# Optimization experiments

Hardware: AMD Instinct MI355X
Metric: run time of the kernel (lower is better)

The kernel has to match this reference:

```python
import jax, jax.numpy as jnp
import numpy as np
from functools import partial

TAU = 2.0          # leak
VTH = 1.0          # threshold_value
DECAY = 1.0 - 1.0 / TAU  # decay_input=False, v_reset=0: v = v*(1-1/tau) + x
PAD = 3
STRIDE = 1


def heaviside(x):
    # forward of spikingjelly surrogate.ATan (surrogate only changes backward)
    return (x >= 0).astype(x.dtype)


def lif(v, inp):
    """One LIF step: charge, fire, hard reset (v_reset=0)."""
    v = v * DECAY + inp
    s = heaviside(v - VTH)
    v = v * (1.0 - s)
    return v, s


def setup_inputs() -> dict:
    key = jax.random.key(0)
    k1, k2, k3, k4 = jax.random.split(key, 4)
    B, L = 64, 2048
    C, H, NC, K = 128, 256, 10, 7
    x = jax.random.normal(k1, (B, L), dtype=jnp.float32)
    conv_w = jax.random.normal(k2, (C, 1, K), dtype=jnp.float32) * (1.0 / np.sqrt(K))
    W1 = jax.random.normal(k3, (H, C), dtype=jnp.float32) * (1.0 / np.sqrt(C))
    W2 = jax.random.normal(k4, (NC, H), dtype=jnp.float32) * (1.0 / np.sqrt(H))
    return {"x": x, "conv_w": conv_w, "W1": W1, "W2": W2}


def _forward(x, conv_w, W1, W2):
    B = x.shape[0]
    C, H, NC = conv_w.shape[0], W1.shape[0], W2.shape[0]
    # Conv1d(1 -> C): [B, 1, L] -> [B, C, T]
    xc = jax.lax.conv_general_dilated(
        x[:, None, :], conv_w, window_strides=(STRIDE,),
        padding=[(PAD, PAD)], dimension_numbers=("NCH", "OIH", "NCH"))
    T = xc.shape[2]
    xt = jnp.transpose(xc, (2, 0, 1))  # [T, B, C]

    def step(carry, x_t):
        v1, v2, v3, acc = carry
        v1, s1 = lif(v1, x_t)                       # conv LIF  [B, C]
        v2, s2 = lif(v2, s1 @ W1.T)                 # hidden LIF [B, H]
        v3, s3 = lif(v3, s2 @ W2.T)                 # output LIF [B, NC]
        return (v1, v2, v3, acc + s3), None

    zeros = lambda d: jnp.zeros((B, d), dtype=x.dtype)
    init = (zeros(C), zeros(H), zeros(NC), zeros(NC))
    (_, _, _, acc), _ = jax.lax.scan(step, init, xt)
    return acc / T


def reference(x, conv_w, W1, W2):
    return _forward(x, conv_w, W1, W2)
```

## Files before the change

### kernel.cpp

```cpp
#include <hip/hip_runtime.h>
#include <stdint.h>

#define T_STEPS 2048
#define BB 64
#define CC 128
#define HH 256
#define NCLS 10

#define S1_OFF  0
#define DP_OFF  2097152
#define DP2_OFF 2228224
#define S2W_OFF 2244608

typedef int v4i __attribute__((ext_vector_type(4)));

__device__ __forceinline__ v4i spread16(unsigned h) {
  v4i a;
  a[0] = (int)((((h      ) & 0xFu) * 0x00204081u) & 0x01010101u);
  a[1] = (int)((((h >> 4 ) & 0xFu) * 0x00204081u) & 0x01010101u);
  a[2] = (int)((((h >> 8 ) & 0xFu) * 0x00204081u) & 0x01010101u);
  a[3] = (int)((((h >> 12) & 0xFu) * 0x00204081u) & 0x01010101u);
  return a;
}

__global__ __launch_bounds__(128) void k01_prep(
    const float* __restrict__ x, const float* __restrict__ cw,
    const float* __restrict__ W1, const float* __restrict__ W2,
    unsigned int* __restrict__ s1b, signed char* __restrict__ dp,
    signed char* __restrict__ dp2, float* __restrict__ out) {
  const int bx = blockIdx.x;
  const int tidx = threadIdx.x;
  __shared__ float xs[200];

  if (bx < 1024) {
    const int c = tidx;
    const int wv = tidx >> 6;
    const int lane = tidx & 63;
    const int b = bx & 63;
    const int t0 = (bx >> 6) * 128;
    const int ts = t0 - 64;

    const float* xb = x + b * 2048;
    const int base = t0 - 67;
    for (int i = tidx; i < 200; i += 128) {
      int l = base + i;
      xs[i] = (l >= 0 && l < 2048) ? xb[l] : 0.0f;
    }
    __syncthreads();

    float w[7];
#pragma unroll
    for (int k = 0; k < 7; ++k) w[k] = cw[c * 7 + k];

    float xw[7];
#pragma unroll
    for (int k = 0; k < 7; ++k) xw[k] = xs[k];

    float v = 0.0f;
#pragma unroll 7
    for (int t = ts; t < t0 + 128; ++t) {
      float u = fmaf(w[0], xw[0],
                fmaf(w[1], xw[1],
                fmaf(w[2], xw[2],
                fmaf(w[3], xw[3],
                fmaf(w[4], xw[4],
                fmaf(w[5], xw[5], w[6] * xw[6]))))));
      v = fmaf(v, 0.5f, u);
      bool sp = (v >= 1.0f);
      unsigned long long Bm = __ballot(sp);
      if (t >= t0 && lane == 0)
        *(unsigned long long*)(s1b + ((size_t)t * BB + b) * 4 + wv * 2) = Bm;
      if (sp) v = 0.0f;
#pragma unroll
      for (int k = 0; k < 6; ++k) xw[k] = xw[k + 1];
      xw[6] = xs[t - t0 + 71];
    }
  } else if (bx < 1280) {
    const int h = bx - 1024;
    const int c = tidx;
    float w = W1[h * CC + c];
    int q = __float2int_rn(w * 2147483648.0f);
#pragma unroll
    for (int d = 0; d < 3; ++d) {
      int dig = (int)(signed char)(q & 0xff);
      dp[d * (HH * CC) + h * CC + c] = (signed char)dig;
      q = (q - dig) >> 8;
    }
    dp[3 * (HH * CC) + h * CC + c] = (signed char)q;
  } else if (bx < 1296) {
    const int nc = bx - 1280;
#pragma unroll
    for (int half = 0; half < 2; ++half) {
      int cc = half * 128 + tidx;
      float w = (nc < NCLS) ? W2[nc * HH + cc] : 0.0f;
      int q = __float2int_rn(w * 2147483648.0f);
#pragma unroll
      for (int d = 0; d < 3; ++d) {
        int dig = (int)(signed char)(q & 0xff);
        dp2[d * (16 * HH) + nc * HH + cc] = (signed char)dig;
        q = (q - dig) >> 8;
      }
      dp2[3 * (16 * HH) + nc * HH + cc] = (signed char)q;
    }
  } else {
#pragma unroll
    for (int i = 0; i < 5; ++i) out[tidx + 128 * i] = 0.0f;
  }
}

__global__ __launch_bounds__(256, 4) void k2_mfma_lif2(
    const unsigned int* __restrict__ s1b, const signed char* __restrict__ dp,
    unsigned int* __restrict__ s2w) {
  const int tid  = threadIdx.x;
  const int lane = tid & 63;
  const int wv   = tid >> 6;
  const int hg   = blockIdx.x;
  const int b    = blockIdx.y;
  const int chunk= blockIdx.z;
  const int t0   = chunk * 256;
  const int nwarm= (chunk == 0) ? 0 : 4;
  const int ts   = t0 - nwarm * 16;
  const int l15  = lane & 15;
  const int lg   = lane >> 4;
  const int nn   = lg >> 1;
  const int hb   = hg * 128 + wv * 32;
  const int hw   = (lg & 1) * 16;

  v4i Bf[2][4][2];
#pragma unroll
  for (int n = 0; n < 2; ++n)
#pragma unroll
    for (int d = 0; d < 4; ++d)
#pragma unroll
      for (int kc = 0; kc < 2; ++kc)
        Bf[n][d][kc] = *(const v4i*)(dp + d * (HH * CC) +
                                     (hb + n * 16 + l15) * CC + kc * 64 + lg * 16);

  const unsigned int* ap = s1b + ((size_t)(ts + l15) * BB + b) * 4;
  uint4 Ra = *(const uint4*)ap;
  uint4 Pb = *(const uint4*)(ap + 16 * BB * 4);
  const unsigned int* ap2 = ap + 2 * 16 * BB * 4;

  const int a4 = l15 * 4;
  float v = 0.0f;
  const v4i ZZ = {0, 0, 0, 0};

  const int nsub = nwarm + 16;
  for (int s = 0; s < nsub; ++s) {
    const int tb = ts + s * 16;

    uint4 Pc = *(const uint4*)ap2;
    ap2 += 16 * BB * 4;

    const unsigned w01 = (lg & 2) ? Ra.y : Ra.x;
    const unsigned w23 = (lg & 2) ? Ra.w : Ra.z;
    v4i Af0 = spread16((w01 >> hw) & 0xFFFFu);
    v4i Af1 = spread16((w23 >> hw) & 0xFFFFu);

    float u0[4], u1[4];
#pragma unroll
    for (int n = 0; n < 2; ++n) {
      v4i a0, a1, a2, a3;
      a0 = __builtin_amdgcn_mfma_i32_16x16x64_i8(Af0, Bf[n][0][0], ZZ, 0, 0, 0);
      a1 = __builtin_amdgcn_mfma_i32_16x16x64_i8(Af0, Bf[n][1][0], ZZ, 0, 0, 0);
      a2 = __builtin_amdgcn_mfma_i32_16x16x64_i8(Af0, Bf[n][2][0], ZZ, 0, 0, 0);
      a3 = __builtin_amdgcn_mfma_i32_16x16x64_i8(Af0, Bf[n][3][0], ZZ, 0, 0, 0);
      a0 = __builtin_amdgcn_mfma_i32_16x16x64_i8(Af1, Bf[n][0][1], a0, 0, 0, 0);
      a1 = __builtin_amdgcn_mfma_i32_16x16x64_i8(Af1, Bf[n][1][1], a1, 0, 0, 0);
      a2 = __builtin_amdgcn_mfma_i32_16x16x64_i8(Af1, Bf[n][2][1], a2, 0, 0, 0);
      a3 = __builtin_amdgcn_mfma_i32_16x16x64_i8(Af1, Bf[n][3][1], a3, 0, 0, 0);
#pragma unroll
      for (int r = 0; r < 4; ++r) {
        int hi = a3[r] * 256 + a2[r];
        int lo = a1[r] * 256 + a0[r];
        float u = fmaf((float)hi, 0x1p-15f, (float)lo * 0x1p-31f);
        if (n == 0) u0[r] = u; else u1[r] = u;
      }
    }

    float ua[16];
#pragma unroll
    for (int q = 0; q < 4; ++q) {
      const int addr = a4 + q * 64;
#pragma unroll
      for (int r = 0; r < 4; ++r) {
        int g0 = __builtin_amdgcn_ds_bpermute(addr, __float_as_int(u0[r]));
        int g1 = __builtin_amdgcn_ds_bpermute(addr, __float_as_int(u1[r]));
        ua[q * 4 + r] = __int_as_float(nn ? g1 : g0);
      }
    }

    unsigned sel = 0;
#define LIFSTEP(J)                                                         \
    {                                                                      \
      v = fmaf(v, 0.5f, ua[J]);                                            \
      bool sp = (v >= 1.0f);                                               \
      if (sp) v = 0.0f;                                                    \
      unsigned long long Bm = __ballot(sp);                                \
      unsigned pk = (unsigned)(Bm & 0xFFFFull) |                           \
                    ((unsigned)((Bm >> 32) & 0xFFFFull) << 16);            \
      asm("v_writelane_b32 %0, %1, " #J : "+v"(sel) : "s"(pk));            \
    }
    LIFSTEP(0)  LIFSTEP(1)  LIFSTEP(2)  LIFSTEP(3)
    LIFSTEP(4)  LIFSTEP(5)  LIFSTEP(6)  LIFSTEP(7)
    LIFSTEP(8)  LIFSTEP(9)  LIFSTEP(10) LIFSTEP(11)
    LIFSTEP(12) LIFSTEP(13) LIFSTEP(14) LIFSTEP(15)
#undef LIFSTEP

    if (s >= nwarm && lg == 0)
      s2w[((size_t)(tb + l15) * BB + b) * 8 + hg * 4 + wv] = sel;

    Ra = Pb; Pb = Pc;
  }
}

__global__ __launch_bounds__(64, 4) void k34_gemm3_lif3(
    const unsigned int* __restrict__ s2w, const signed char* __restrict__ dp2,
    float* __restrict__ out) {
  const int lane = threadIdx.x;
  const int l15  = lane & 15;
  const int lg   = lane >> 4;
  const int b    = blockIdx.x;
  const int chunk= blockIdx.y;
  const int t0   = chunk * 32;
  const int nwarm= (chunk == 0) ? 0 : 4;
  const int ts   = t0 - nwarm * 16;

  v4i Bf[4][4];
#pragma unroll
  for (int d = 0; d < 4; ++d)
#pragma unroll
    for (int kc = 0; kc < 4; ++kc)
      Bf[d][kc] = *(const v4i*)(dp2 + d * (16 * HH) + l15 * HH + kc * 64 + lg * 16);

  const uint4* rp = (const uint4*)s2w + ((size_t)(ts + l15) * BB + b) * 2;
  uint4 r0 = rp[0], r1 = rp[1];
  rp += 16 * BB * 2;

  const int a4 = l15 * 4;
  const int hw = (lg & 1) * 16;
  float v = 0.0f, cnt = 0.0f;
  const v4i ZZ = {0, 0, 0, 0};

  const int nsub = nwarm + 2;
  for (int s = 0; s < nsub; ++s) {
    uint4 p0 = rp[0], p1 = rp[1];
    rp += 16 * BB * 2;

    unsigned rowd[8] = {r0.x, r0.y, r0.z, r0.w, r1.x, r1.y, r1.z, r1.w};

    v4i a0, a1, a2, a3;
#pragma unroll
    for (int kc = 0; kc < 4; ++kc) {
      unsigned h16 = (rowd[kc * 2 + (lg >> 1)] >> hw) & 0xFFFFu;
      v4i Af = spread16(h16);
      a0 = __builtin_amdgcn_mfma_i32_16x16x64_i8(Af, Bf[0][kc], kc ? a0 : ZZ, 0, 0, 0);
      a1 = __builtin_amdgcn_mfma_i32_16x16x64_i8(Af, Bf[1][kc], kc ? a1 : ZZ, 0, 0, 0);
      a2 = __builtin_amdgcn_mfma_i32_16x16x64_i8(Af, Bf[2][kc], kc ? a2 : ZZ, 0, 0, 0);
      a3 = __builtin_amdgcn_mfma_i32_16x16x64_i8(Af, Bf[3][kc], kc ? a3 : ZZ, 0, 0, 0);
    }

    float u[4];
#pragma unroll
    for (int r = 0; r < 4; ++r) {
      int hi = a3[r] * 256 + a2[r];
      int lo = a1[r] * 256 + a0[r];
      u[r] = fmaf((float)hi, 0x1p-15f, (float)lo * 0x1p-31f);
    }

    float ua[16];
#pragma unroll
    for (int q = 0; q < 4; ++q) {
      const int addr = a4 + q * 64;
#pragma unroll
      for (int r = 0; r < 4; ++r)
        ua[q * 4 + r] = __int_as_float(
            __builtin_amdgcn_ds_bpermute(addr, __float_as_int(u[r])));
    }

    float inc = (s >= nwarm) ? 1.0f : 0.0f;
#pragma unroll
    for (int j = 0; j < 16; ++j) {
      v = fmaf(v, 0.5f, ua[j]);
      bool sp = (v >= 1.0f);
      if (sp) { v = 0.0f; cnt += inc; }
    }

    r0 = p0; r1 = p1;
  }

  if (lane < NCLS)
    atomicAdd(&out[b * NCLS + lane], cnt * (1.0f / 2048.0f));
}

extern "C" void kernel_launch(void* const* d_in, const int* in_sizes, int n_in,
                              void* d_out, int out_size, void* d_ws, size_t ws_size,
                              hipStream_t stream) {
  const float* x  = (const float*)d_in[0];
  const float* cw = (const float*)d_in[1];
  const float* W1 = (const float*)d_in[2];
  const float* W2 = (const float*)d_in[3];
  float* out = (float*)d_out;

  char* ws = (char*)d_ws;
  unsigned int*  s1b = (unsigned int*)(ws + S1_OFF);
  signed char*   dp  = (signed char*)(ws + DP_OFF);
  signed char*   dp2 = (signed char*)(ws + DP2_OFF);
  unsigned int*  s2w = (unsigned int*)(ws + S2W_OFF);

  k01_prep<<<dim3(1297), 128, 0, stream>>>(x, cw, W1, W2, s1b, dp, dp2, out);
  k2_mfma_lif2<<<dim3(2, 64, 8), 256, 0, stream>>>(s1b, dp, s2w);
  k34_gemm3_lif3<<<dim3(64, 64), 64, 0, stream>>>(s2w, dp2, out);
  (void)in_sizes; (void)n_in; (void)out_size; (void)ws_size;
}
```

Measured before the change: 144.9 us.

## Have each k2 block cover all 256 hidden units, doubling per-wave work

Removes the hidden-group grid dimension so each block covers all 256 hidden units, with each wave handling 64 units (4 MFMA n-tiles instead of 2). Each time step's spike A-fragments are loaded and expanded once per batch row instead of twice, and the grid shrinks by half. The spike-word packing changes from writelane of 16-bit halves to per-lane 32-bit ballot words, written by two lane groups. Register pressure doubles for the weight fragments (launch bounds drop to 2 blocks), so occupancy and latency hiding fall, and the grid of 512 blocks may underfill the device.

```diff
diff --git a/kernel.cpp b/kernel.cpp
--- a/kernel.cpp
+++ b/kernel.cpp
@@ -108,27 +108,27 @@
   }
 }
 
-__global__ __launch_bounds__(256, 4) void k2_mfma_lif2(
+__global__ __launch_bounds__(256, 2) void k2_mfma_lif2(
     const unsigned int* __restrict__ s1b, const signed char* __restrict__ dp,
     unsigned int* __restrict__ s2w) {
   const int tid  = threadIdx.x;
   const int lane = tid & 63;
   const int wv   = tid >> 6;
-  const int hg   = blockIdx.x;
-  const int b    = blockIdx.y;
-  const int chunk= blockIdx.z;
+  const int b    = blockIdx.x;
+  const int chunk= blockIdx.y;
   const int t0   = chunk * 256;
   const int nwarm= (chunk == 0) ? 0 : 4;
   const int ts   = t0 - nwarm * 16;
   const int l15  = lane & 15;
   const int lg   = lane >> 4;
-  const int nn   = lg >> 1;
-  const int hb   = hg * 128 + wv * 32;
+  const int hb   = wv * 64;
   const int hw   = (lg & 1) * 16;
-
-  v4i Bf[2][4][2];
-#pragma unroll
-  for (int n = 0; n < 2; ++n)
+  const bool c1  = (lg & 1) != 0;
+  const bool c2  = (lg & 2) != 0;
+
+  v4i Bf[4][4][2];
+#pragma unroll
+  for (int n = 0; n < 4; ++n)
 #pragma unroll
     for (int d = 0; d < 4; ++d)
 #pragma unroll
@@ -157,9 +157,9 @@
     v4i Af0 = spread16((w01 >> hw) & 0xFFFFu);
     v4i Af1 = spread16((w23 >> hw) & 0xFFFFu);
 
-    float u0[4], u1[4];
-#pragma unroll
-    for (int n = 0; n < 2; ++n) {
+    float u[4][4];
+#pragma unroll
+    for (int n = 0; n < 4; ++n) {
       v4i a0, a1, a2, a3;
       a0 = __builtin_amdgcn_mfma_i32_16x16x64_i8(Af0, Bf[n][0][0], ZZ, 0, 0, 0);
       a1 = __builtin_amdgcn_mfma_i32_16x16x64_i8(Af0, Bf[n][1][0], ZZ, 0, 0, 0);
@@ -173,8 +173,7 @@
       for (int r = 0; r < 4; ++r) {
         int hi = a3[r] * 256 + a2[r];
         int lo = a1[r] * 256 + a0[r];
-        float u = fmaf((float)hi, 0x1p-15f, (float)lo * 0x1p-31f);
-        if (n == 0) u0[r] = u; else u1[r] = u;
+        u[n][r] = fmaf((float)hi, 0x1p-15f, (float)lo * 0x1p-31f);
       }
     }
 
@@ -184,31 +183,29 @@
       const int addr = a4 + q * 64;
 #pragma unroll
       for (int r = 0; r < 4; ++r) {
-        int g0 = __builtin_amdgcn_ds_bpermute(addr, __float_as_int(u0[r]));
-        int g1 = __builtin_amdgcn_ds_bpermute(addr, __float_as_int(u1[r]));
-        ua[q * 4 + r] = __int_as_float(nn ? g1 : g0);
+        int g0 = __builtin_amdgcn_ds_bpermute(addr, __float_as_int(u[0][r]));
+        int g1 = __builtin_amdgcn_ds_bpermute(addr, __float_as_int(u[1][r]));
+        int g2 = __builtin_amdgcn_ds_bpermute(addr, __float_as_int(u[2][r]));
+        int g3 = __builtin_amdgcn_ds_bpermute(addr, __float_as_int(u[3][r]));
+        int sA = c2 ? g2 : g0;
+        int sB = c2 ? g3 : g1;
+        ua[q * 4 + r] = __int_as_float(c1 ? sB : sA);
       }
     }
 
     unsigned sel = 0;
-#define LIFSTEP(J)                                                         \
-    {                                                                      \
-      v = fmaf(v, 0.5f, ua[J]);                                            \
-      bool sp = (v >= 1.0f);                                               \
-      if (sp) v = 0.0f;                                                    \
-      unsigned long long Bm = __ballot(sp);                                \
-      unsigned pk = (unsigned)(Bm & 0xFFFFull) |                           \
-                    ((unsigned)((Bm >> 32) & 0xFFFFull) << 16);            \
-      asm("v_writelane_b32 %0, %1, " #J : "+v"(sel) : "s"(pk));            \
-    }
-    LIFSTEP(0)  LIFSTEP(1)  LIFSTEP(2)  LIFSTEP(3)
-    LIFSTEP(4)  LIFSTEP(5)  LIFSTEP(6)  LIFSTEP(7)
-    LIFSTEP(8)  LIFSTEP(9)  LIFSTEP(10) LIFSTEP(11)
-    LIFSTEP(12) LIFSTEP(13) LIFSTEP(14) LIFSTEP(15)
-#undef LIFSTEP
-
-    if (s >= nwarm && lg == 0)
-      s2w[((size_t)(tb + l15) * BB + b) * 8 + hg * 4 + wv] = sel;
+#pragma unroll
+    for (int j = 0; j < 16; ++j) {
+      v = fmaf(v, 0.5f, ua[j]);
+      bool sp = (v >= 1.0f);
+      if (sp) v = 0.0f;
+      unsigned long long Bm = __ballot(sp);
+      unsigned pk = c1 ? (unsigned)(Bm >> 32) : (unsigned)Bm;
+      if (l15 == j) sel = pk;
+    }
+
+    if (s >= nwarm && lg < 2)
+      s2w[((size_t)(tb + l15) * BB + b) * 8 + wv * 2 + lg] = sel;
 
     Ra = Pb; Pb = Pc;
   }
@@ -309,7 +306,7 @@
   unsigned int*  s2w = (unsigned int*)(ws + S2W_OFF);
 
   k01_prep<<<dim3(1297), 128, 0, stream>>>(x, cw, W1, W2, s1b, dp, dp2, out);
-  k2_mfma_lif2<<<dim3(2, 64, 8), 256, 0, stream>>>(s1b, dp, s2w);
+  k2_mfma_lif2<<<dim3(64, 8), 256, 0, stream>>>(s1b, dp, s2w);
   k34_gemm3_lif3<<<dim3(64, 64), 64, 0, stream>>>(s2w, dp2, out);
   (void)in_sizes; (void)n_in; (void)out_size; (void)ws_size;
 }
```

Result: slower. 148.2 us (+2.3%).
